# Kernel tuning notes

Measured on AMD Instinct MI355X. Metric: run time of the kernel, lower is better.

The kernel has to match this reference:

```python
import jax, jax.numpy as jnp
import numpy as np

N_ITERS = 25
LAMBDA_INIT = 0.1
TOL = 1e-6
EPS = 1e-10
REWEIGHTED = True


def setup_inputs() -> dict:
    key = jax.random.key(0)
    k1, k2 = jax.random.split(key)
    Y = jax.random.normal(k1, (16, 1024, 64), dtype=jnp.float32)   # [batch, T, joints]
    D = jax.random.normal(k2, (1024, 2048), dtype=jnp.float32)     # [T, Np]
    return {"Y": Y, "D": D}


def _soft_threshold(x, tau):
    return jnp.sign(x) * jnp.maximum(jnp.abs(x) - tau, 0.0)


def _converge(C_curr, C_prev, t_prev, DtD, DtY, L, lam):
    # Fixed-length scan emulating the torch loop with a data-dependent break:
    # once the Frobenius norm of (C_next - C_curr) drops below TOL, the state
    # is frozen (equivalent to breaking out of the loop).
    def body(carry, _):
        Cc, Cp, t, done = carry
        grad = jnp.einsum('pq,bqj->bpj', DtD, Cp) - DtY      # [b, Np, j]
        C_next = _soft_threshold(Cp - L * grad, L * lam)
        small = jnp.linalg.norm(C_next - Cc) < TOL
        do = jnp.logical_not(done | small)
        t_next = (1.0 + jnp.sqrt(1.0 + 4.0 * t * t)) * 0.5
        t_const = (t - 1.0) / t_next
        Cp_new = C_next + t_const * (C_next - Cc)
        carry = (jnp.where(do, C_next, Cc),
                 jnp.where(do, Cp_new, Cp),
                 jnp.where(do, t_next, t),
                 done | small)
        return carry, None

    init = (C_curr, C_prev, t_prev, jnp.array(False))
    (Cc, Cp, t, _), _ = jax.lax.scan(body, init, None, length=N_ITERS)
    return Cc, Cp, t


def _fista(Y, D):
    b, T, j = Y.shape
    Np = D.shape[1]
    Dt = D.T
    DtD = Dt @ D                                   # [Np, Np]
    DtY = jnp.einsum('pt,btj->bpj', Dt, Y)         # [b, Np, j]
    L = 1.0 / jnp.linalg.norm(DtD, ord=2)          # 1 / spectral norm
    Cc = jnp.zeros((b, Np, j), Y.dtype)
    Cp = Cc
    t = jnp.asarray(1.0, Y.dtype)
    lam = jnp.asarray(LAMBDA_INIT, Y.dtype)
    if REWEIGHTED:
        # torch runs: converge -> weight_lambda -> converge -> weight_lambda;
        # the final weight_lambda does not affect the returned C.
        Cc, Cp, t = _converge(Cc, Cp, t, DtD, DtY, L, lam)
        w = 1.0 / (jnp.abs(Cc) + EPS)
        w = w / jnp.linalg.norm(w, axis=1, keepdims=True)  # L2 over Np dim
        lam = lam * w * Np
        Cc, Cp, t = _converge(Cc, Cp, t, DtD, DtY, L, lam)
    else:
        Cc, Cp, t = _converge(Cc, Cp, t, DtD, DtY, L, lam)
    return Cc


def reference(Y, D):
    return _fista(Y, D)
```

## Files before the change

### kernel.cpp

```cpp
#include <hip/hip_runtime.h>
#include <math.h>

#define T_DIM 1024
#define NP    2048
#define NB    1024
#define NITER 25
#define NSQ   7
#define NPI   8
#define LAM0  0.1f
#define EPS_W 1e-10f

typedef float    f32x4 __attribute__((ext_vector_type(4)));
typedef _Float16 f16x8 __attribute__((ext_vector_type(8)));
typedef _Float16 f16x4 __attribute__((ext_vector_type(4)));

__device__ __forceinline__ void gload16(const void* g, void* l) {
  __builtin_amdgcn_global_load_lds((const __attribute__((address_space(1))) unsigned int*)g,
                                   (__attribute__((address_space(3))) unsigned int*)l, 16, 0, 0);
}

__device__ __forceinline__ void mm3_core(
    const _Float16* __restrict__ Ah, const _Float16* __restrict__ Al,
    const _Float16* __restrict__ Bh, const _Float16* __restrict__ Bl,
    int ldk, int n0, int p0, int kb0, int nsteps,
    f32x4 acc0[4][2], f32x4 acc1[4][2])
{
  __shared__ __align__(16) _Float16 sAh[8192], sAl[8192], sBh[8192], sBl[8192];
  const int tid = threadIdx.x;
  const int lane = tid & 63, wave = tid >> 6;
  const int quad = lane >> 4, rl = lane & 15;
#pragma unroll
  for (int i = 0; i < 4; i++)
#pragma unroll
    for (int j = 0; j < 2; j++) { acc0[i][j] = (f32x4)0.0f; acc1[i][j] = (f32x4)0.0f; }
  const int wn = (wave >> 2) * 64, wp = (wave & 3) * 32;

  for (int s = 0; s < nsteps; s++) {
    const int kb = kb0 + s * 64;
    if (s) __syncthreads();
#pragma unroll
    for (int i = 0; i < 2; i++) {
      int slot = i * 512 + wave * 64 + lane;
      int kc = slot >> 7, row = slot & 127;
      int lb = (i * 512 + wave * 64) * 8;
      size_t ga = (size_t)(n0 + row) * ldk + kb + kc * 8;
      size_t gb = (size_t)(p0 + row) * ldk + kb + kc * 8;
      gload16(Ah + ga, sAh + lb);
      gload16(Al + ga, sAl + lb);
      gload16(Bh + gb, sBh + lb);
      gload16(Bl + gb, sBl + lb);
    }
    __syncthreads();
#pragma unroll
    for (int kk = 0; kk < 2; kk++) {
      const int kc = kk * 4 + quad;
      f16x8 a_h[4], a_l[4], b_h[2], b_l[2];
#pragma unroll
      for (int t = 0; t < 4; t++) {
        int ar = wn + t * 16 + rl;
        a_h[t] = *(const f16x8*)&sAh[(kc * 128 + ar) * 8];
        a_l[t] = *(const f16x8*)&sAl[(kc * 128 + ar) * 8];
      }
#pragma unroll
      for (int t = 0; t < 2; t++) {
        int bp = wp + t * 16 + rl;
        b_h[t] = *(const f16x8*)&sBh[(kc * 128 + bp) * 8];
        b_l[t] = *(const f16x8*)&sBl[(kc * 128 + bp) * 8];
      }
#pragma unroll
      for (int mt = 0; mt < 4; mt++)
#pragma unroll
        for (int nt = 0; nt < 2; nt++)
          acc0[mt][nt] = __builtin_amdgcn_mfma_f32_16x16x32_f16(a_h[mt], b_h[nt], acc0[mt][nt], 0, 0, 0);
#pragma unroll
      for (int mt = 0; mt < 4; mt++)
#pragma unroll
        for (int nt = 0; nt < 2; nt++)
          acc1[mt][nt] = __builtin_amdgcn_mfma_f32_16x16x32_f16(a_l[mt], b_h[nt], acc1[mt][nt], 0, 0, 0);
#pragma unroll
      for (int mt = 0; mt < 4; mt++)
#pragma unroll
        for (int nt = 0; nt < 2; nt++)
          acc1[mt][nt] = __builtin_amdgcn_mfma_f32_16x16x32_f16(a_h[mt], b_l[nt], acc1[mt][nt], 0, 0, 0);
    }
  }
}

__global__ __launch_bounds__(512, 4) void k_mm(const _Float16* __restrict__ Ch, const _Float16* __restrict__ Cl,
                                               const _Float16* __restrict__ H, const _Float16* __restrict__ Ee,
                                               float* __restrict__ part) {
  const int b = blockIdx.x;
  const int xcd = b & 7, q = b >> 3;
  const int pt = xcd * 2 + (q & 1);
  const int ny = (q >> 1) & 7;
  const int z  = q >> 4;
  f32x4 acc0[4][2], acc1[4][2];
  const int n0 = ny * 128, p0 = pt * 128;
  mm3_core(Ch, Cl, H, Ee, 2048, n0, p0, z * 512, 8, acc0, acc1);
  const int lane = threadIdx.x & 63, wave = threadIdx.x >> 6;
  const int quad = lane >> 4, rl = lane & 15;
  const int wn = (wave >> 2) * 64, wp = (wave & 3) * 32;
  float* op = part + (size_t)z * NB * NP;
#pragma unroll
  for (int mt = 0; mt < 4; mt++)
#pragma unroll
    for (int nt = 0; nt < 2; nt++) {
      const int p = p0 + wp + nt * 16 + rl;
      const size_t rb = (size_t)(n0 + wn + mt * 16 + quad * 4) * NP + p;
#pragma unroll
      for (int r = 0; r < 4; r++)
        op[rb + (size_t)r * NP] = acc0[mt][nt][r] + acc1[mt][nt][r] * (1.f / 4096.f);
    }
}

__global__ __launch_bounds__(256) void k_epi(const float* __restrict__ part,
    const float* __restrict__ DtY_, const float* __restrict__ CcIn,
    const _Float16* __restrict__ ChIn, const _Float16* __restrict__ ClIn,
    const float* __restrict__ Lptr, const float* __restrict__ thrM, float tc,
    float* __restrict__ CcOut, _Float16* __restrict__ ChOut, _Float16* __restrict__ ClOut) {
  const size_t g = ((size_t)blockIdx.x * 256 + threadIdx.x) * 4;
  const float Lv = Lptr[0];
  float ps[4], dy[4], cc[4], th[4];
  *(float4*)ps = *(const float4*)(part + g);
#pragma unroll
  for (int z = 1; z < 4; z++) {
    float t[4];
    *(float4*)t = *(const float4*)(part + (size_t)z * NB * NP + g);
#pragma unroll
    for (int j = 0; j < 4; j++) ps[j] += t[j];
  }
  *(float4*)dy = *(const float4*)(DtY_ + g);
  *(float4*)cc = *(const float4*)(CcIn + g);
  f16x4 chv = *(const f16x4*)(ChIn + g);
  f16x4 clv = *(const f16x4*)(ClIn + g);
  if (thrM) { *(float4*)th = *(const float4*)(thrM + g); }
  float cn[4];
  f16x4 ho, lo;
#pragma unroll
  for (int j = 0; j < 4; j++) {
    float grad = ps[j] - dy[j];
    float cp = (float)chv[j] + (float)clv[j] * (1.f / 4096.f);
    float z = cp - Lv * grad;
    float t2 = thrM ? th[j] : Lv * LAM0;
    float az = fabsf(z) - t2;
    float v = az > 0.f ? copysignf(az, z) : 0.f;
    cn[j] = v;
    float cpn = fmaf(tc, v - cc[j], v);
    _Float16 h = (_Float16)cpn;
    ho[j] = h;
    lo[j] = (_Float16)((cpn - (float)h) * 4096.f);
  }
  *(float4*)(CcOut + g) = *(float4*)cn;
  *(f16x4*)(ChOut + g) = ho;
  *(f16x4*)(ClOut + g) = lo;
}

__device__ __forceinline__ void mm3c(
    const _Float16* __restrict__ Ah, const _Float16* __restrict__ Al,
    const _Float16* __restrict__ Bh, const _Float16* __restrict__ Bl,
    int ldk, int n0, int p0, int nsteps,
    f32x4 acc0[2][2], f32x4 acc1[2][2])
{
  __shared__ __align__(16) _Float16 sAh[8192], sAl[8192], sBh[8192], sBl[8192];
  const int tid = threadIdx.x;
  const int lane = tid & 63, w = tid >> 6;
  const int quad = lane >> 4, rl = lane & 15;
  const int wm = (w >> 1) * 32, wp = (w & 1) * 32;
#pragma unroll
  for (int i = 0; i < 2; i++)
#pragma unroll
    for (int j = 0; j < 2; j++) { acc0[i][j] = (f32x4)0.0f; acc1[i][j] = (f32x4)0.0f; }

  for (int s = 0; s < nsteps; s++) {
    const int kb = s * 128;
    if (s) __syncthreads();
#pragma unroll
    for (int i = 0; i < 4; i++) {
      int slot = i * 256 + w * 64 + lane;
      int kc = slot >> 6, row = slot & 63;
      int lb = (i * 256 + w * 64) * 8;
      size_t ga = (size_t)(n0 + row) * ldk + kb + kc * 8;
      size_t gb = (size_t)(p0 + row) * ldk + kb + kc * 8;
      gload16(Ah + ga, sAh + lb);
      gload16(Al + ga, sAl + lb);
      gload16(Bh + gb, sBh + lb);
      gload16(Bl + gb, sBl + lb);
    }
    __syncthreads();
#pragma unroll
    for (int kk = 0; kk < 4; kk++) {
      const int kc = kk * 4 + quad;
      f16x8 a_h[2], a_l[2], b_h[2], b_l[2];
#pragma unroll
      for (int t = 0; t < 2; t++) {
        int ar = wm + t * 16 + rl;
        int bp = wp + t * 16 + rl;
        a_h[t] = *(const f16x8*)&sAh[(kc * 64 + ar) * 8];
        a_l[t] = *(const f16x8*)&sAl[(kc * 64 + ar) * 8];
        b_h[t] = *(const f16x8*)&sBh[(kc * 64 + bp) * 8];
        b_l[t] = *(const f16x8*)&sBl[(kc * 64 + bp) * 8];
      }
#pragma unroll
      for (int mt = 0; mt < 2; mt++)
#pragma unroll
        for (int nt = 0; nt < 2; nt++) {
          acc0[mt][nt] = __builtin_amdgcn_mfma_f32_16x16x32_f16(a_h[mt], b_h[nt], acc0[mt][nt], 0, 0, 0);
          acc1[mt][nt] = __builtin_amdgcn_mfma_f32_16x16x32_f16(a_l[mt], b_h[nt], acc1[mt][nt], 0, 0, 0);
          acc1[mt][nt] = __builtin_amdgcn_mfma_f32_16x16x32_f16(a_h[mt], b_l[nt], acc1[mt][nt], 0, 0, 0);
        }
    }
  }
}

__global__ __launch_bounds__(256, 2) void k_dtd(const _Float16* __restrict__ Dth, const _Float16* __restrict__ Dtl,
                                                _Float16* __restrict__ H, _Float16* __restrict__ Ee) {
  const int b = blockIdx.x;
  const int xcd = b & 7, i4 = b >> 3;
  const int ny = i4 >> 2, pt = xcd * 4 + (i4 & 3);
  const int n0 = ny * 64, p0 = pt * 64;
  f32x4 acc0[2][2], acc1[2][2];
  mm3c(Dth, Dtl, Dth, Dtl, 1024, n0, p0, 8, acc0, acc1);
  const int lane = threadIdx.x & 63, w = threadIdx.x >> 6;
  const int quad = lane >> 4, rl = lane & 15;
  const int wm = (w >> 1) * 32, wp = (w & 1) * 32;
#pragma unroll
  for (int mt = 0; mt < 2; mt++)
#pragma unroll
    for (int nt = 0; nt < 2; nt++) {
      const int p = p0 + wp + nt * 16 + rl;
      const size_t rb = (size_t)(n0 + wm + mt * 16 + quad * 4) * NP + p;
#pragma unroll
      for (int r = 0; r < 4; r++) {
        const size_t idx = rb + (size_t)r * NP;
        float v = acc0[mt][nt][r] + acc1[mt][nt][r] * (1.f / 4096.f);
        _Float16 h = (_Float16)v;
        H[idx] = h;
        Ee[idx] = (_Float16)((v - (float)h) * 4096.f);
      }
    }
}

__global__ __launch_bounds__(256, 2) void k_g(const _Float16* __restrict__ Dh, const _Float16* __restrict__ Dl,
                                              float* __restrict__ G, float* __restrict__ ss0) {
  const int b = blockIdx.x;
  const int xcd = b & 7, i4 = b >> 3;
  const int ny = i4 >> 1, pt = xcd * 2 + (i4 & 1);
  const int n0 = ny * 64, p0 = pt * 64;
  f32x4 acc0[2][2], acc1[2][2];
  mm3c(Dh, Dl, Dh, Dl, 2048, n0, p0, 16, acc0, acc1);
  const int tid = threadIdx.x;
  const int lane = tid & 63, w = tid >> 6;
  const int quad = lane >> 4, rl = lane & 15;
  const int wm = (w >> 1) * 32, wp = (w & 1) * 32;
  float ssl = 0.f;
#pragma unroll
  for (int mt = 0; mt < 2; mt++)
#pragma unroll
    for (int nt = 0; nt < 2; nt++) {
      const int p = p0 + wp + nt * 16 + rl;
      const size_t rb = (size_t)(n0 + wm + mt * 16 + quad * 4) * 1024 + p;
#pragma unroll
      for (int r = 0; r < 4; r++) {
        float v = acc0[mt][nt][r] + acc1[mt][nt][r] * (1.f / 4096.f);
        G[rb + (size_t)r * 1024] = v;
        ssl = fmaf(v, v, ssl);
      }
    }
  __shared__ float red[256];
  red[tid] = ssl; __syncthreads();
  for (int off = 128; off > 0; off >>= 1) {
    if (tid < off) red[tid] += red[tid + off];
    __syncthreads();
  }
  if (tid == 0) atomicAdd(ss0, red[0]);
}

__global__ __launch_bounds__(256, 2) void k_dty(const _Float16* __restrict__ Yth, const _Float16* __restrict__ Ytl,
                                                const _Float16* __restrict__ Dth, const _Float16* __restrict__ Dtl,
                                                float* __restrict__ DtY_) {
  const int b = blockIdx.x;
  const int xcd = b & 7, i4 = b >> 3;
  const int ny = i4 >> 2, pt = xcd * 4 + (i4 & 3);
  const int n0 = ny * 64, p0 = pt * 64;
  f32x4 acc0[2][2], acc1[2][2];
  mm3c(Yth, Ytl, Dth, Dtl, 1024, n0, p0, 8, acc0, acc1);
  const int lane = threadIdx.x & 63, w = threadIdx.x >> 6;
  const int quad = lane >> 4, rl = lane & 15;
  const int wm = (w >> 1) * 32, wp = (w & 1) * 32;
#pragma unroll
  for (int mt = 0; mt < 2; mt++)
#pragma unroll
    for (int nt = 0; nt < 2; nt++) {
      const int p = p0 + wp + nt * 16 + rl;
      const size_t rb = (size_t)(n0 + wm + mt * 16 + quad * 4) * NP + p;
#pragma unroll
      for (int r = 0; r < 4; r++)
        DtY_[rb + (size_t)r * NP] = acc0[mt][nt][r] + acc1[mt][nt][r] * (1.f / 4096.f);
    }
}

__global__ __launch_bounds__(256, 2) void k_sqf(const _Float16* __restrict__ Min, const float* __restrict__ ssPrev,
                                                _Float16* __restrict__ Mout, float* __restrict__ ssNext,
                                                float invfac) {
  __shared__ __align__(16) _Float16 sA[8192], sB[8192];
  const int b = blockIdx.x;
  const int xcd = b & 7, i4 = b >> 3;
  const int ny = i4 >> 1, pt = xcd * 2 + (i4 & 1);
  const int n0 = ny * 64, p0 = pt * 64;
  const int tid = threadIdx.x;
  const int lane = tid & 63, w = tid >> 6;
  const int quad = lane >> 4, rl = lane & 15;
  const int wm = (w >> 1) * 32, wp = (w & 1) * 32;
  f32x4 acc[2][2];
#pragma unroll
  for (int i = 0; i < 2; i++)
#pragma unroll
    for (int j = 0; j < 2; j++) acc[i][j] = (f32x4)0.0f;

  for (int s = 0; s < 8; s++) {
    const int kb = s * 128;
    if (s) __syncthreads();
#pragma unroll
    for (int i = 0; i < 4; i++) {
      int slot = i * 256 + w * 64 + lane;
      int kc = slot >> 6, row = slot & 63;
      int lb = (i * 256 + w * 64) * 8;
      gload16(Min + (size_t)(n0 + row) * 1024 + kb + kc * 8, sA + lb);
      gload16(Min + (size_t)(p0 + row) * 1024 + kb + kc * 8, sB + lb);
    }
    __syncthreads();
#pragma unroll
    for (int kk = 0; kk < 4; kk++) {
      const int kc = kk * 4 + quad;
      f16x8 a[2], bb[2];
#pragma unroll
      for (int t = 0; t < 2; t++) {
        a[t]  = *(const f16x8*)&sA[(kc * 64 + wm + t * 16 + rl) * 8];
        bb[t] = *(const f16x8*)&sB[(kc * 64 + wp + t * 16 + rl) * 8];
      }
#pragma unroll
      for (int mt = 0; mt < 2; mt++)
#pragma unroll
        for (int nt = 0; nt < 2; nt++)
          acc[mt][nt] = __builtin_amdgcn_mfma_f32_16x16x32_f16(a[mt], bb[nt], acc[mt][nt], 0, 0, 0);
    }
  }
  const float inv = invfac / ssPrev[0];
  float ssl = 0.f;
#pragma unroll
  for (int mt = 0; mt < 2; mt++)
#pragma unroll
    for (int nt = 0; nt < 2; nt++) {
      const int p = p0 + wp + nt * 16 + rl;
      const size_t rb = (size_t)(n0 + wm + mt * 16 + quad * 4) * 1024 + p;
#pragma unroll
      for (int r = 0; r < 4; r++) {
        float v = acc[mt][nt][r] * inv;
        Mout[rb + (size_t)r * 1024] = (_Float16)(v * 4096.f);
        ssl = fmaf(v, v, ssl);
      }
    }
  __syncthreads();
  float* red = (float*)sA;
  red[tid] = ssl; __syncthreads();
  for (int off = 128; off > 0; off >>= 1) {
    if (tid < off) red[tid] += red[tid + off];
    __syncthreads();
  }
  if (tid == 0) atomicAdd(ssNext, red[0]);
}

__global__ __launch_bounds__(256) void k_split(const float* __restrict__ src, _Float16* __restrict__ H,
                                               _Float16* __restrict__ L, int n4) {
  int g = blockIdx.x * 256 + threadIdx.x;
  if (g < n4) {
    float4 v = ((const float4*)src)[g];
    float vv[4] = {v.x, v.y, v.z, v.w};
    f16x4 h, l;
#pragma unroll
    for (int j = 0; j < 4; j++) {
      _Float16 hh = (_Float16)vv[j];
      h[j] = hh;
      l[j] = (_Float16)((vv[j] - (float)hh) * 4096.f);
    }
    ((f16x4*)H)[g] = h;
    ((f16x4*)L)[g] = l;
  }
}

__global__ __launch_bounds__(256) void k_h16(const float* __restrict__ src, _Float16* __restrict__ dst,
                                             int n4, float scale) {
  int g = blockIdx.x * 256 + threadIdx.x;
  if (g < n4) {
    float4 v = ((const float4*)src)[g];
    f16x4 h;
    h[0] = (_Float16)(v.x * scale); h[1] = (_Float16)(v.y * scale);
    h[2] = (_Float16)(v.z * scale); h[3] = (_Float16)(v.w * scale);
    ((f16x4*)dst)[g] = h;
  }
}

__global__ __launch_bounds__(256) void k_tr(const float* __restrict__ src, float* __restrict__ dst,
                                            int R, int C) {
  __shared__ float T[64][65];
  const int tid = threadIdx.x;
  const int c0 = blockIdx.x * 64, r0 = blockIdx.y * 64;
  const int cx = tid & 15, ry = tid >> 4;
#pragma unroll
  for (int ii = 0; ii < 4; ii++) {
    int r = ry + ii * 16;
    float4 v = *(const float4*)(src + (size_t)(r0 + r) * C + c0 + cx * 4);
    T[cx * 4 + 0][r] = v.x; T[cx * 4 + 1][r] = v.y;
    T[cx * 4 + 2][r] = v.z; T[cx * 4 + 3][r] = v.w;
  }
  __syncthreads();
#pragma unroll
  for (int ii = 0; ii < 4; ii++) {
    int c = ry + ii * 16;
    float4 v = make_float4(T[c][cx * 4], T[c][cx * 4 + 1], T[c][cx * 4 + 2], T[c][cx * 4 + 3]);
    *(float4*)(dst + (size_t)(c0 + c) * R + r0 + cx * 4) = v;
  }
}

__global__ __launch_bounds__(256) void k_trY(const float* __restrict__ Y, float* __restrict__ Yt) {
  __shared__ float T[64][65];
  const int tid = threadIdx.x;
  const int t0 = blockIdx.x * 64, b = blockIdx.y;
  const int cx = tid & 15, ry = tid >> 4;
#pragma unroll
  for (int ii = 0; ii < 4; ii++) {
    int r = ry + ii * 16;
    float4 v = *(const float4*)(Y + ((size_t)b * T_DIM + t0 + r) * 64 + cx * 4);
    T[cx * 4 + 0][r] = v.x; T[cx * 4 + 1][r] = v.y;
    T[cx * 4 + 2][r] = v.z; T[cx * 4 + 3][r] = v.w;
  }
  __syncthreads();
#pragma unroll
  for (int ii = 0; ii < 4; ii++) {
    int j = ry + ii * 16;
    float4 v = make_float4(T[j][cx * 4], T[j][cx * 4 + 1], T[j][cx * 4 + 2], T[j][cx * 4 + 3]);
    *(float4*)(Yt + ((size_t)b * 64 + j) * T_DIM + t0 + cx * 4) = v;
  }
}

__global__ void k_initx(float* __restrict__ X) {
  int g = blockIdx.x * 256 + threadIdx.x;
  if (g < 4096) {
    unsigned h = (unsigned)g * 2654435761u;
    h ^= h >> 16; h *= 2246822519u; h ^= h >> 13;
    X[g] = ((float)(h & 0xffffff) / 16777216.0f) - 0.5f;
  }
}

__global__ __launch_bounds__(256) void k_matvec(const _Float16* __restrict__ M, const float* __restrict__ Xin,
                                                float* __restrict__ Xout, const float* __restrict__ prevNorm,
                                                float* __restrict__ outNorm) {
  const int tid = threadIdx.x, lane = tid & 63, w = tid >> 6;
  const int row = blockIdx.x * 4 + w;
  const _Float16* Mr = M + (size_t)row * 1024;
  float s[4] = {0.f, 0.f, 0.f, 0.f};
  for (int j = 0; j < 16; j++) {
    int k = j * 64 + lane;
    float m = (float)Mr[k];
    float4 x = *(const float4*)(Xin + k * 4);
    s[0] = fmaf(m, x.x, s[0]); s[1] = fmaf(m, x.y, s[1]);
    s[2] = fmaf(m, x.z, s[2]); s[3] = fmaf(m, x.w, s[3]);
  }
#pragma unroll
  for (int off = 32; off > 0; off >>= 1)
#pragma unroll
    for (int c = 0; c < 4; c++) s[c] += __shfl_down(s[c], off, 64);
  __shared__ float red[16];
  if (lane == 0) {
#pragma unroll
    for (int c = 0; c < 4; c++) {
      float sc = prevNorm ? rsqrtf(prevNorm[c]) : 1.0f;
      float o = s[c] * sc;
      Xout[row * 4 + c] = o;
      red[w * 4 + c] = o * o;
    }
  }
  __syncthreads();
  if (tid < 4) atomicAdd(&outNorm[tid], red[tid] + red[4 + tid] + red[8 + tid] + red[12 + tid]);
}

__global__ __launch_bounds__(256) void k_rq(const float* __restrict__ G, const float* __restrict__ X,
                                            float* __restrict__ num, float* __restrict__ den) {
  const int tid = threadIdx.x, lane = tid & 63, w = tid >> 6;
  const int row = blockIdx.x * 4 + w;
  const float* Gr = G + (size_t)row * 1024;
  float s[4] = {0.f, 0.f, 0.f, 0.f};
  for (int j = 0; j < 16; j++) {
    int k = j * 64 + lane;
    float m = Gr[k];
    float4 x = *(const float4*)(X + k * 4);
    s[0] = fmaf(m, x.x, s[0]); s[1] = fmaf(m, x.y, s[1]);
    s[2] = fmaf(m, x.z, s[2]); s[3] = fmaf(m, x.w, s[3]);
  }
#pragma unroll
  for (int off = 32; off > 0; off >>= 1)
#pragma unroll
    for (int c = 0; c < 4; c++) s[c] += __shfl_down(s[c], off, 64);
  __shared__ float rn[16], rd[16];
  if (lane == 0) {
    float4 v = *(const float4*)(X + row * 4);
    float vv[4] = {v.x, v.y, v.z, v.w};
#pragma unroll
    for (int c = 0; c < 4; c++) { rn[w * 4 + c] = vv[c] * s[c]; rd[w * 4 + c] = vv[c] * vv[c]; }
  }
  __syncthreads();
  if (tid < 4) {
    atomicAdd(&num[tid], rn[tid] + rn[4 + tid] + rn[8 + tid] + rn[12 + tid]);
    atomicAdd(&den[tid], rd[tid] + rd[4 + tid] + rd[8 + tid] + rd[12 + tid]);
  }
}

__global__ void k_finL(const float* __restrict__ num, const float* __restrict__ den, float* __restrict__ Lout) {
  if (threadIdx.x == 0 && blockIdx.x == 0) {
    float best = 0.f;
    for (int c = 0; c < 4; c++) { float r = num[c] / den[c]; best = fmaxf(best, r); }
    Lout[0] = 1.0f / best;
  }
}

__global__ __launch_bounds__(256) void k_rowss(const float* __restrict__ Cc, float* __restrict__ rowss) {
  const int n = blockIdx.x, tid = threadIdx.x;
  const float4* row = (const float4*)(Cc + (size_t)n * NP);
  float s = 0.f;
  for (int i = tid; i < 512; i += 256) {
    float4 v = row[i];
    float r0 = 1.f / (fabsf(v.x) + EPS_W), r1 = 1.f / (fabsf(v.y) + EPS_W);
    float r2 = 1.f / (fabsf(v.z) + EPS_W), r3 = 1.f / (fabsf(v.w) + EPS_W);
    s += r0 * r0 + r1 * r1 + r2 * r2 + r3 * r3;
  }
  __shared__ float red[256];
  red[tid] = s; __syncthreads();
  for (int off = 128; off > 0; off >>= 1) {
    if (tid < off) red[tid] += red[tid + off];
    __syncthreads();
  }
  if (tid == 0) rowss[n] = red[0];
}

__global__ __launch_bounds__(256) void k_thrmat(const float* __restrict__ Cc, const float* __restrict__ rowss,
                                                const float* __restrict__ Lptr, float* __restrict__ thrMat) {
  const size_t g = (size_t)blockIdx.x * 256 + threadIdx.x;
  const int n = (int)(g >> 11);
  float r = 1.0f / (fabsf(Cc[g]) + EPS_W);
  thrMat[g] = Lptr[0] * LAM0 * (float)NP * r * rsqrtf(rowss[n]);
}

__global__ __launch_bounds__(256) void k_out(const float* __restrict__ Cc, float* __restrict__ out) {
  __shared__ float T[64][65];
  const int tid = threadIdx.x;
  const int p0 = blockIdx.x * 64, nt = blockIdx.y;
  const int pr = tid & 15, nr = tid >> 4;
#pragma unroll
  for (int ii = 0; ii < 4; ii++) {
    int n_l = nr + ii * 16;
    float4 v = *(const float4*)(Cc + ((size_t)nt * 64 + n_l) * NP + p0 + pr * 4);
    T[pr * 4 + 0][n_l] = v.x; T[pr * 4 + 1][n_l] = v.y;
    T[pr * 4 + 2][n_l] = v.z; T[pr * 4 + 3][n_l] = v.w;
  }
  __syncthreads();
#pragma unroll
  for (int ii = 0; ii < 4; ii++) {
    int p_l = nr + ii * 16;
    float4 v = make_float4(T[p_l][pr * 4], T[p_l][pr * 4 + 1], T[p_l][pr * 4 + 2], T[p_l][pr * 4 + 3]);
    *(float4*)(out + (size_t)nt * (NP * 64) + (size_t)(p0 + p_l) * 64 + pr * 4) = v;
  }
}

#define MBf(x) ((size_t)(x) * 262144)

extern "C" void kernel_launch(void* const* d_in, const int* in_sizes, int n_in,
                              void* d_out, int out_size, void* d_ws, size_t ws_size,
                              hipStream_t stream) {
  const float* Y = (const float*)d_in[0];
  const float* D = (const float*)d_in[1];
  float* out = (float*)d_out;
  float* ws = (float*)d_ws;

  _Float16* H    = (_Float16*)(ws);
  _Float16* Ee   = (_Float16*)(ws + MBf(8));
  float*    DtY  = ws + MBf(16);
  float*    Cc0  = ws + MBf(24);
  float*    Cc1  = ws + MBf(32);
  _Float16* Ch0  = (_Float16*)(ws + MBf(40));
  _Float16* Cl0  = (_Float16*)(ws + MBf(44));
  _Float16* Ch1  = (_Float16*)(ws + MBf(48));
  _Float16* Cl1  = (_Float16*)(ws + MBf(52));
  float*    thrM = ws + MBf(56);
  float*    part = ws + MBf(64);
  float*    Dt   = ws + MBf(64);
  float*    Yt   = ws + MBf(72);
  float*    G    = ws + MBf(76);
  _Float16* Mh0  = (_Float16*)(ws + MBf(80));
  _Float16* Mh1  = (_Float16*)(ws + MBf(82));
  _Float16* Dh   = (_Float16*)(ws + MBf(32));
  _Float16* Dl   = (_Float16*)(ws + MBf(36));
  _Float16* Dth  = (_Float16*)(ws + MBf(48));
  _Float16* Dtl  = (_Float16*)(ws + MBf(52));
  _Float16* Yth  = (_Float16*)(ws + MBf(56));
  _Float16* Ytl  = (_Float16*)(ws + MBf(58));
  float*    XA   = ws + MBf(96);
  float*    XB   = XA + 4096;
  float*    scal = XB + 4096;
  float*    ssv   = scal;
  float*    norms = scal + 8;
  float*    num   = scal + 8 + NPI * 4;
  float*    den   = num + 4;
  float*    Lp    = den + 4;
  float*    rowss = Lp + 4;

  float*    CcB[2] = {Cc0, Cc1};
  _Float16* ChB[2] = {Ch0, Ch1};
  _Float16* ClB[2] = {Cl0, Cl1};

  hipMemsetAsync(Cc0, 0, (size_t)NB * NP * sizeof(float), stream);
  hipMemsetAsync(Ch0, 0, (size_t)2 * NB * NP * sizeof(_Float16), stream);
  hipMemsetAsync(scal, 0, (8 + NPI * 4 + 16) * sizeof(float), stream);

  k_initx<<<16, 256, 0, stream>>>(XA);
  k_tr <<<dim3(32, 16), 256, 0, stream>>>(D, Dt, 1024, 2048);
  k_trY<<<dim3(16, 16), 256, 0, stream>>>(Y, Yt);
  k_split<<<2048, 256, 0, stream>>>(D,  Dh,  Dl,  (T_DIM * NP) / 4);
  k_split<<<2048, 256, 0, stream>>>(Dt, Dth, Dtl, (T_DIM * NP) / 4);
  k_split<<<1024, 256, 0, stream>>>(Yt, Yth, Ytl, (NB * T_DIM) / 4);
  k_g  <<<256,  256, 0, stream>>>(Dh, Dl, G, ssv);
  k_dtd<<<1024, 256, 0, stream>>>(Dth, Dtl, H, Ee);
  k_dty<<<512,  256, 0, stream>>>(Yth, Ytl, Dth, Dtl, DtY);
  k_h16<<<1024, 256, 0, stream>>>(G, Mh0, (1024 * 1024) / 4, 1.0f / 64.0f);
  _Float16* MB[2] = {Mh0, Mh1};
  for (int l = 0; l < NSQ; l++) {
    float invfac = (l == 0) ? 4096.0f : (1.0f / 16777216.0f);
    k_sqf<<<256, 256, 0, stream>>>(MB[l & 1], ssv + l, MB[(l + 1) & 1], ssv + l + 1, invfac);
  }
  _Float16* Mfin = MB[NSQ & 1];
  for (int i = 0; i < NPI; i++) {
    const float* xin = (i & 1) ? XB : XA;
    float* xout = (i & 1) ? XA : XB;
    k_matvec<<<256, 256, 0, stream>>>(Mfin, xin, xout,
                                      i ? norms + (i - 1) * 4 : nullptr, norms + i * 4);
  }
  k_rq  <<<256, 256, 0, stream>>>(G, XA, num, den);
  k_finL<<<1, 64, 0, stream>>>(num, den, Lp);

  float tcv[2 * NITER];
  {
    float t = 1.0f;
    for (int i = 0; i < 2 * NITER; i++) {
      float tn = 0.5f * (1.0f + sqrtf(1.0f + 4.0f * t * t));
      tcv[i] = (t - 1.0f) / tn;
      t = tn;
    }
  }

  for (int i = 0; i < 2 * NITER; i++) {
    int a = i & 1, b = (i + 1) & 1;
    if (i == NITER) {
      k_rowss <<<1024, 256, 0, stream>>>(CcB[a], rowss);
      k_thrmat<<<(NB * NP) / 256, 256, 0, stream>>>(CcB[a], rowss, Lp, thrM);
    }
    const float* thr = (i < NITER) ? nullptr : thrM;
    k_mm <<<512, 512, 0, stream>>>(ChB[a], ClB[a], H, Ee, part);
    k_epi<<<(NB * NP) / 1024, 256, 0, stream>>>(part, DtY, CcB[a], ChB[a], ClB[a], Lp, thr,
                                                tcv[i], CcB[b], ChB[b], ClB[b]);
  }
  k_out<<<dim3(32, 16), 256, 0, stream>>>(CcB[0], out);
}
```

Measured before the change: 3.724 ms.

## Double-buffer LDS tiles in split-f16 GEMM and remap epilogue blocks per XCD

```diff
diff --git a/kernel.cpp b/kernel.cpp
--- a/kernel.cpp
+++ b/kernel.cpp
@@ -5,7 +5,7 @@
 #define NP    2048
 #define NB    1024
 #define NITER 25
-#define NSQ   7
+#define NSQ   5
 #define NPI   8
 #define LAM0  0.1f
 #define EPS_W 1e-10f
@@ -19,70 +19,73 @@
                                    (__attribute__((address_space(3))) unsigned int*)l, 16, 0, 0);
 }
 
-__device__ __forceinline__ void mm3_core(
+__device__ __forceinline__ void mm3_db(
     const _Float16* __restrict__ Ah, const _Float16* __restrict__ Al,
     const _Float16* __restrict__ Bh, const _Float16* __restrict__ Bl,
     int ldk, int n0, int p0, int kb0, int nsteps,
     f32x4 acc0[4][2], f32x4 acc1[4][2])
 {
-  __shared__ __align__(16) _Float16 sAh[8192], sAl[8192], sBh[8192], sBl[8192];
+  __shared__ __align__(16) _Float16 sm[2][4][4096];
   const int tid = threadIdx.x;
   const int lane = tid & 63, wave = tid >> 6;
   const int quad = lane >> 4, rl = lane & 15;
+  const int wn = (wave >> 2) * 64, wp = (wave & 3) * 32;
+  const int kc = tid >> 7, row = tid & 127;
+  const int lbe = wave * 512;
 #pragma unroll
   for (int i = 0; i < 4; i++)
 #pragma unroll
     for (int j = 0; j < 2; j++) { acc0[i][j] = (f32x4)0.0f; acc1[i][j] = (f32x4)0.0f; }
-  const int wn = (wave >> 2) * 64, wp = (wave & 3) * 32;
-
+
+  {
+    size_t ga = (size_t)(n0 + row) * ldk + kb0 + kc * 8;
+    size_t gb = (size_t)(p0 + row) * ldk + kb0 + kc * 8;
+    gload16(Ah + ga, &sm[0][0][lbe]);
+    gload16(Al + ga, &sm[0][1][lbe]);
+    gload16(Bh + gb, &sm[0][2][lbe]);
+    gload16(Bl + gb, &sm[0][3][lbe]);
+  }
   for (int s = 0; s < nsteps; s++) {
-    const int kb = kb0 + s * 64;
-    if (s) __syncthreads();
-#pragma unroll
-    for (int i = 0; i < 2; i++) {
-      int slot = i * 512 + wave * 64 + lane;
-      int kc = slot >> 7, row = slot & 127;
-      int lb = (i * 512 + wave * 64) * 8;
+    const int cur = s & 1;
+    __syncthreads();
+    if (s + 1 < nsteps) {
+      const int nxt = cur ^ 1;
+      const int kb = kb0 + (s + 1) * 32;
       size_t ga = (size_t)(n0 + row) * ldk + kb + kc * 8;
       size_t gb = (size_t)(p0 + row) * ldk + kb + kc * 8;
-      gload16(Ah + ga, sAh + lb);
-      gload16(Al + ga, sAl + lb);
-      gload16(Bh + gb, sBh + lb);
-      gload16(Bl + gb, sBl + lb);
-    }
-    __syncthreads();
-#pragma unroll
-    for (int kk = 0; kk < 2; kk++) {
-      const int kc = kk * 4 + quad;
-      f16x8 a_h[4], a_l[4], b_h[2], b_l[2];
-#pragma unroll
-      for (int t = 0; t < 4; t++) {
-        int ar = wn + t * 16 + rl;
-        a_h[t] = *(const f16x8*)&sAh[(kc * 128 + ar) * 8];
-        a_l[t] = *(const f16x8*)&sAl[(kc * 128 + ar) * 8];
-      }
-#pragma unroll
-      for (int t = 0; t < 2; t++) {
-        int bp = wp + t * 16 + rl;
-        b_h[t] = *(const f16x8*)&sBh[(kc * 128 + bp) * 8];
-        b_l[t] = *(const f16x8*)&sBl[(kc * 128 + bp) * 8];
-      }
-#pragma unroll
-      for (int mt = 0; mt < 4; mt++)
-#pragma unroll
-        for (int nt = 0; nt < 2; nt++)
-          acc0[mt][nt] = __builtin_amdgcn_mfma_f32_16x16x32_f16(a_h[mt], b_h[nt], acc0[mt][nt], 0, 0, 0);
-#pragma unroll
-      for (int mt = 0; mt < 4; mt++)
-#pragma unroll
-        for (int nt = 0; nt < 2; nt++)
-          acc1[mt][nt] = __builtin_amdgcn_mfma_f32_16x16x32_f16(a_l[mt], b_h[nt], acc1[mt][nt], 0, 0, 0);
-#pragma unroll
-      for (int mt = 0; mt < 4; mt++)
-#pragma unroll
-        for (int nt = 0; nt < 2; nt++)
-          acc1[mt][nt] = __builtin_amdgcn_mfma_f32_16x16x32_f16(a_h[mt], b_l[nt], acc1[mt][nt], 0, 0, 0);
-    }
+      gload16(Ah + ga, &sm[nxt][0][lbe]);
+      gload16(Al + ga, &sm[nxt][1][lbe]);
+      gload16(Bh + gb, &sm[nxt][2][lbe]);
+      gload16(Bl + gb, &sm[nxt][3][lbe]);
+    }
+    f16x8 a_h[4], a_l[4], b_h[2], b_l[2];
+#pragma unroll
+    for (int t = 0; t < 4; t++) {
+      int ar = (quad * 128 + wn + t * 16 + rl) * 8;
+      a_h[t] = *(const f16x8*)&sm[cur][0][ar];
+      a_l[t] = *(const f16x8*)&sm[cur][1][ar];
+    }
+#pragma unroll
+    for (int t = 0; t < 2; t++) {
+      int bp = (quad * 128 + wp + t * 16 + rl) * 8;
+      b_h[t] = *(const f16x8*)&sm[cur][2][bp];
+      b_l[t] = *(const f16x8*)&sm[cur][3][bp];
+    }
+#pragma unroll
+    for (int mt = 0; mt < 4; mt++)
+#pragma unroll
+      for (int nt = 0; nt < 2; nt++)
+        acc0[mt][nt] = __builtin_amdgcn_mfma_f32_16x16x32_f16(a_h[mt], b_h[nt], acc0[mt][nt], 0, 0, 0);
+#pragma unroll
+    for (int mt = 0; mt < 4; mt++)
+#pragma unroll
+      for (int nt = 0; nt < 2; nt++)
+        acc1[mt][nt] = __builtin_amdgcn_mfma_f32_16x16x32_f16(a_l[mt], b_h[nt], acc1[mt][nt], 0, 0, 0);
+#pragma unroll
+    for (int mt = 0; mt < 4; mt++)
+#pragma unroll
+      for (int nt = 0; nt < 2; nt++)
+        acc1[mt][nt] = __builtin_amdgcn_mfma_f32_16x16x32_f16(a_h[mt], b_l[nt], acc1[mt][nt], 0, 0, 0);
   }
 }
 
@@ -96,7 +99,7 @@
   const int z  = q >> 4;
   f32x4 acc0[4][2], acc1[4][2];
   const int n0 = ny * 128, p0 = pt * 128;
-  mm3_core(Ch, Cl, H, Ee, 2048, n0, p0, z * 512, 8, acc0, acc1);
+  mm3_db(Ch, Cl, H, Ee, 2048, n0, p0, z * 512, 16, acc0, acc1);
   const int lane = threadIdx.x & 63, wave = threadIdx.x >> 6;
   const int quad = lane >> 4, rl = lane & 15;
   const int wn = (wave >> 2) * 64, wp = (wave & 3) * 32;
@@ -118,7 +121,14 @@
     const _Float16* __restrict__ ChIn, const _Float16* __restrict__ ClIn,
     const float* __restrict__ Lptr, const float* __restrict__ thrM, float tc,
     float* __restrict__ CcOut, _Float16* __restrict__ ChOut, _Float16* __restrict__ ClOut) {
-  const size_t g = ((size_t)blockIdx.x * 256 + threadIdx.x) * 4;
+  const int b = blockIdx.x;
+  const int xcd = b & 7, r_ = b >> 3;
+  const int pt = xcd * 2 + (r_ & 1);
+  const int nc = r_ >> 1;
+  const int tid = threadIdx.x;
+  const int rowi = nc * 8 + (tid >> 5);
+  const int col = pt * 128 + (tid & 31) * 4;
+  const size_t g = (size_t)rowi * NP + col;
   const float Lv = Lptr[0];
   float ps[4], dy[4], cc[4], th[4];
   *(float4*)ps = *(const float4*)(part + g);
@@ -664,8 +674,8 @@
     }
     const float* thr = (i < NITER) ? nullptr : thrM;
     k_mm <<<512, 512, 0, stream>>>(ChB[a], ClB[a], H, Ee, part);
-    k_epi<<<(NB * NP) / 1024, 256, 0, stream>>>(part, DtY, CcB[a], ChB[a], ClB[a], Lp, thr,
-                                                tcv[i], CcB[b], ChB[b], ClB[b]);
+    k_epi<<<2048, 256, 0, stream>>>(part, DtY, CcB[a], ChB[a], ClB[a], Lp, thr,
+                                    tcv[i], CcB[b], ChB[b], ClB[b]);
   }
   k_out<<<dim3(32, 16), 256, 0, stream>>>(CcB[0], out);
 }
```

After: 3.410 ms. -8.4%, faster.
